# Kernel tuning notes

Hardware: AMD Instinct MI355X
Metric: run time of the kernel (lower is better)

Reference implementation:

```python
import jax, jax.numpy as jnp
import numpy as np

N = 50000      # nodes
E = 800000     # edges
IN = 128       # in_dim
EMB = 32       # emb_dim
ED = 8         # edge_dim
L = 4          # num_layers
B = 64         # num graphs in batch
OUT = 10       # out_dim
EPS = 1e-5


def setup_inputs() -> dict:
    key = jax.random.key(0)
    ks = jax.random.split(key, 16)
    f32 = jnp.float32
    def nrm(k, shape, scale):
        return jax.random.normal(k, shape, dtype=f32) * scale
    inp = {}
    inp['x'] = nrm(ks[0], (N, IN), 1.0)
    inp['edge_index'] = jax.random.randint(ks[1], (2, E), 0, N)
    inp['edge_attr'] = nrm(ks[2], (E, ED), 1.0)
    inp['batch'] = jnp.sort(jax.random.randint(ks[3], (N,), 0, B))
    # lin_in
    inp['lin_in_w'] = nrm(ks[4], (IN, EMB), 0.05)
    inp['lin_in_b'] = jnp.zeros((EMB,), f32)
    # per-layer message MLP: Linear(2e+ed->e), BN, ReLU, Linear(e->e), BN, ReLU
    inp['msg_w1'] = nrm(ks[5], (L, 2 * EMB + ED, EMB), 0.1)
    inp['msg_b1'] = jnp.zeros((L, EMB), f32)
    inp['msg_g1'] = jnp.ones((L, EMB), f32)
    inp['msg_be1'] = jnp.zeros((L, EMB), f32)
    inp['msg_w2'] = nrm(ks[6], (L, EMB, EMB), 0.1)
    inp['msg_b2'] = jnp.zeros((L, EMB), f32)
    inp['msg_g2'] = jnp.ones((L, EMB), f32)
    inp['msg_be2'] = jnp.zeros((L, EMB), f32)
    # per-layer update MLP: Linear(2e->e), BN, ReLU, Linear(e->e), BN, ReLU
    inp['upd_w1'] = nrm(ks[7], (L, 2 * EMB, EMB), 0.1)
    inp['upd_b1'] = jnp.zeros((L, EMB), f32)
    inp['upd_g1'] = jnp.ones((L, EMB), f32)
    inp['upd_be1'] = jnp.zeros((L, EMB), f32)
    inp['upd_w2'] = nrm(ks[8], (L, EMB, EMB), 0.1)
    inp['upd_b2'] = jnp.zeros((L, EMB), f32)
    inp['upd_g2'] = jnp.ones((L, EMB), f32)
    inp['upd_be2'] = jnp.zeros((L, EMB), f32)
    # lin_pred
    inp['pred_w'] = nrm(ks[9], (EMB, OUT), 0.1)
    inp['pred_b'] = jnp.zeros((OUT,), f32)
    return inp


def _bn(x, g, b):
    # BatchNorm1d in training mode: batch stats over dim 0 (biased variance)
    mu = jnp.mean(x, axis=0)
    var = jnp.mean(jnp.square(x - mu), axis=0)
    return (x - mu) * jax.lax.rsqrt(var + EPS) * g + b


def reference(x, edge_attr, lin_in_w, lin_in_b,
              msg_w1, msg_b1, msg_g1, msg_be1, msg_w2, msg_b2, msg_g2, msg_be2,
              upd_w1, upd_b1, upd_g1, upd_be1, upd_w2, upd_b2, upd_g2, upd_be2,
              pred_w, pred_b, edge_index, batch):
    src = edge_index[0]  # h_j source nodes
    dst = edge_index[1]  # h_i target nodes (aggregation index)
    h = x @ lin_in_w + lin_in_b  # [N, EMB]
    for i in range(L):
        # message: gather + concat + MLP(BN,ReLU)x2 over edges
        msg_in = jnp.concatenate([h[dst], h[src], edge_attr], axis=-1)  # [E, 2e+ed]
        m = jax.nn.relu(_bn(msg_in @ msg_w1[i] + msg_b1[i], msg_g1[i], msg_be1[i]))
        m = jax.nn.relu(_bn(m @ msg_w2[i] + msg_b2[i], msg_g2[i], msg_be2[i]))
        # aggregate: scatter-add by destination
        aggr = jax.ops.segment_sum(m, dst, num_segments=N)  # [N, EMB]
        # update: concat + MLP(BN,ReLU)x2
        u = jnp.concatenate([h, aggr], axis=-1)  # [N, 2e]
        u = jax.nn.relu(_bn(u @ upd_w1[i] + upd_b1[i], upd_g1[i], upd_be1[i]))
        u = jax.nn.relu(_bn(u @ upd_w2[i] + upd_b2[i], upd_g2[i], upd_be2[i]))
        h = u + h  # residual in MPNNModel.get_embeddings
    # global mean pool
    sums = jax.ops.segment_sum(h, batch, num_segments=B)
    counts = jax.ops.segment_sum(jnp.ones((N,), h.dtype), batch, num_segments=B)
    h_graph = sums / jnp.maximum(counts, 1.0)[:, None]
    return h_graph @ pred_w + pred_b  # [B, OUT]
```

## Files before the change

kernel.cpp:

```cpp
#include <hip/hip_runtime.h>
#include <cstddef>

#define N_NODES 50000
#define N_EDGES 800000
#define IN_DIM  128
#define EMB     32
#define ED      8
#define NLAYERS 4
#define NB      64
#define OUTD    10
#define EPS_BN  1e-5f

#define EDGE_GRID 3125
#define NODE_GRID 196
#define NODE4_GRID 782
#define AGGR_GRID 6250
#define MSG1_EPT  2
#define MSG1_GRID 1563
#define NT16      50000
#define MSG2_TPW  16
#define MSG2_GRID 782

#define SREP 4

typedef short bf16x8 __attribute__((ext_vector_type(8)));
typedef float f32x4  __attribute__((ext_vector_type(4)));


__device__ __forceinline__ unsigned short f2bf(float x) {
  union { float f; unsigned u; } v; v.f = x;
  unsigned b = v.u + 0x7FFFu + ((v.u >> 16) & 1u);
  return (unsigned short)(b >> 16);
}
__device__ __forceinline__ float bf2f(unsigned short s) {
  union { unsigned u; float f; } v; v.u = ((unsigned)s) << 16;
  return v.f;
}

__device__ __forceinline__ uint4 pack8_bf16(const float v[8]) {
  uint4 o;
  o.x = (unsigned)f2bf(v[0]) | ((unsigned)f2bf(v[1]) << 16);
  o.y = (unsigned)f2bf(v[2]) | ((unsigned)f2bf(v[3]) << 16);
  o.z = (unsigned)f2bf(v[4]) | ((unsigned)f2bf(v[5]) << 16);
  o.w = (unsigned)f2bf(v[6]) | ((unsigned)f2bf(v[7]) << 16);
  return o;
}

__device__ __forceinline__ void mac8_f4(float acc[8], const float4 v, const float* __restrict__ wk) {
#pragma unroll
  for (int j = 0; j < 8; ++j) acc[j] = fmaf(v.x, wk[j], acc[j]);
#pragma unroll
  for (int j = 0; j < 8; ++j) acc[j] = fmaf(v.y, wk[EMB + j], acc[j]);
#pragma unroll
  for (int j = 0; j < 8; ++j) acc[j] = fmaf(v.z, wk[2*EMB + j], acc[j]);
#pragma unroll
  for (int j = 0; j < 8; ++j) acc[j] = fmaf(v.w, wk[3*EMB + j], acc[j]);
}

__device__ __forceinline__ void coef_from_stats(const float* __restrict__ stats_stage,
                                                const float* __restrict__ g,
                                                const float* __restrict__ be,
                                                float inv_count, float* __restrict__ cf) {
  if (threadIdx.x < EMB) {
    const int c = threadIdx.x;
    float s = 0.f, ss = 0.f;
#pragma unroll
    for (int r = 0; r < SREP; ++r) {
      s  += stats_stage[r*64 + c];
      ss += stats_stage[r*64 + EMB + c];
    }
    const float mu  = s * inv_count;
    const float var = ss * inv_count - mu*mu;
    const float a = g[c] * rsqrtf(var + EPS_BN);
    cf[c] = a;
    cf[EMB + c] = fmaf(-mu, a, be[c]);
  }
  __syncthreads();
}

__device__ __forceinline__ void wave_stats_atomic(float ts[8], float tss[8],
                                                  float* __restrict__ lds_s,
                                                  float* __restrict__ lds_q,
                                                  float* __restrict__ stats_stage) {
  const int lane = threadIdx.x & 63;
  const int wv   = threadIdx.x >> 6;
#pragma unroll
  for (int j = 0; j < 8; ++j) {
    float a = ts[j], b = tss[j];
#pragma unroll
    for (int o = 32; o > 0; o >>= 1) {
      a += __shfl_down(a, o, 64);
      b += __shfl_down(b, o, 64);
    }
    ts[j] = a; tss[j] = b;
  }
  if (lane == 0) {
#pragma unroll
    for (int j = 0; j < 8; ++j) {
      lds_s[wv*8 + j] = ts[j];
      lds_q[wv*8 + j] = tss[j];
    }
  }
  __syncthreads();
  if (threadIdx.x < 64) {
    const float v = (threadIdx.x < 32) ? lds_s[threadIdx.x] : lds_q[threadIdx.x - 32];
    atomicAdd(stats_stage + ((blockIdx.x & (SREP-1)) << 6) + threadIdx.x, v);
  }
}

__device__ __forceinline__ void block_stats_atomic(const float ts[EMB], const float tss[EMB],
                                                   float* __restrict__ stats_stage) {
  __shared__ float sred[256];
  const int lane = threadIdx.x & 63;
  const int wid  = threadIdx.x >> 6;
#pragma unroll
  for (int c = 0; c < EMB; ++c) {
    float a = ts[c];
    float q = tss[c];
#pragma unroll
    for (int o = 32; o > 0; o >>= 1) {
      a += __shfl_down(a, o, 64);
      q += __shfl_down(q, o, 64);
    }
    if (lane == 0) { sred[wid*64 + c] = a; sred[wid*64 + EMB + c] = q; }
  }
  __syncthreads();
  if (threadIdx.x < 64) {
    const float v = sred[threadIdx.x] + sred[64 + threadIdx.x] +
                    sred[128 + threadIdx.x] + sred[192 + threadIdx.x];
    atomicAdd(stats_stage + ((blockIdx.x & (SREP-1)) << 6) + threadIdx.x, v);
  }
}


__global__ __launch_bounds__(256) void k_lin_in_pq(
    const float* __restrict__ x, const float* __restrict__ w, const float* __restrict__ b,
    const float* __restrict__ w1, const float* __restrict__ b1,
    float* __restrict__ h, unsigned short* __restrict__ p, unsigned short* __restrict__ q)
{
  __shared__ float lds_h[64][33];
  const int lane = threadIdx.x & 63;
  const int wv   = threadIdx.x >> 6;
  const int n  = blockIdx.x*64 + lane;
  const int c0 = wv*8;
  if (n < N_NODES) {
    float acc[8];
#pragma unroll
    for (int j = 0; j < 8; ++j) acc[j] = b[c0 + j];
    const float4* xp = (const float4*)(x + (size_t)n*IN_DIM);
#pragma unroll 8
    for (int k4 = 0; k4 < IN_DIM/4; ++k4)
      mac8_f4(acc, xp[k4], w + (k4*4)*EMB + c0);
    float4 o0, o1;
    o0.x = acc[0]; o0.y = acc[1]; o0.z = acc[2]; o0.w = acc[3];
    o1.x = acc[4]; o1.y = acc[5]; o1.z = acc[6]; o1.w = acc[7];
    *(float4*)(h + (size_t)n*EMB + c0)     = o0;
    *(float4*)(h + (size_t)n*EMB + c0 + 4) = o1;
#pragma unroll
    for (int j = 0; j < 8; ++j) lds_h[lane][c0 + j] = acc[j];
  }
  __syncthreads();
  if (n < N_NODES) {
    float ap[8], aq[8];
#pragma unroll
    for (int j = 0; j < 8; ++j) { ap[j] = b1[c0 + j]; aq[j] = 0.f; }
#pragma unroll
    for (int k = 0; k < EMB; ++k) {
      const float hv = lds_h[lane][k];
      const float* wp = w1 + k*EMB + c0;
      const float* wq = w1 + (EMB + k)*EMB + c0;
#pragma unroll
      for (int j = 0; j < 8; ++j) ap[j] = fmaf(hv, wp[j], ap[j]);
#pragma unroll
      for (int j = 0; j < 8; ++j) aq[j] = fmaf(hv, wq[j], aq[j]);
    }
    *(uint4*)(p + (size_t)n*EMB + c0) = pack8_bf16(ap);
    *(uint4*)(q + (size_t)n*EMB + c0) = pack8_bf16(aq);
  }
}

__global__ __launch_bounds__(256) void k_upd1(
    const float* __restrict__ h, float* __restrict__ aggr,
    const float* __restrict__ w, const float* __restrict__ b,
    float* __restrict__ stats)
{
  __shared__ float lds_s[32], lds_q[32];
  const int lane = threadIdx.x & 63;
  const int wv   = threadIdx.x >> 6;
  const int n  = blockIdx.x*64 + lane;
  const int c0 = wv*8;
  float acc[8];
#pragma unroll
  for (int j = 0; j < 8; ++j) acc[j] = 0.f;
  if (n < N_NODES) {
#pragma unroll
    for (int j = 0; j < 8; ++j) acc[j] = b[c0 + j];
    const float4* hp = (const float4*)(h + (size_t)n*EMB);
    const float4* ap = (const float4*)(aggr + (size_t)n*EMB);
#pragma unroll
    for (int k4 = 0; k4 < 8; ++k4) mac8_f4(acc, hp[k4], w + (k4*4)*EMB + c0);
#pragma unroll
    for (int k4 = 0; k4 < 8; ++k4) mac8_f4(acc, ap[k4], w + (EMB + k4*4)*EMB + c0);
  }
  float ts[8], tss[8];
#pragma unroll
  for (int j = 0; j < 8; ++j) { ts[j] = acc[j]; tss[j] = acc[j]*acc[j]; }
  wave_stats_atomic(ts, tss, lds_s, lds_q, stats);
  if (n < N_NODES) {
    float4 o0, o1;
    o0.x = acc[0]; o0.y = acc[1]; o0.z = acc[2]; o0.w = acc[3];
    o1.x = acc[4]; o1.y = acc[5]; o1.z = acc[6]; o1.w = acc[7];
    *(float4*)(aggr + (size_t)n*EMB + c0)     = o0;
    *(float4*)(aggr + (size_t)n*EMB + c0 + 4) = o1;
  }
}

__global__ __launch_bounds__(256) void k_upd2(
    float* __restrict__ z,
    const float* __restrict__ stats1, const float* __restrict__ g1, const float* __restrict__ be1,
    const float* __restrict__ w, const float* __restrict__ b,
    float* __restrict__ stats2)
{
  __shared__ float cf[64];
  __shared__ float lds_s[32], lds_q[32];
  coef_from_stats(stats1, g1, be1, 1.0f/(float)N_NODES, cf);

  const int lane = threadIdx.x & 63;
  const int wv   = threadIdx.x >> 6;
  const int n  = blockIdx.x*64 + lane;
  const int c0 = wv*8;
  float acc[8];
#pragma unroll
  for (int j = 0; j < 8; ++j) acc[j] = 0.f;
  if (n < N_NODES) {
#pragma unroll
    for (int j = 0; j < 8; ++j) acc[j] = b[c0 + j];
    const float4* zp = (const float4*)(z + (size_t)n*EMB);
#pragma unroll
    for (int k4 = 0; k4 < 8; ++k4) {
      const float4 v = zp[k4];
      const float mv[4] = {v.x, v.y, v.z, v.w};
#pragma unroll
      for (int t = 0; t < 4; ++t) {
        const int k = 4*k4 + t;
        const float m = fmaxf(fmaf(cf[k], mv[t], cf[EMB + k]), 0.f);
        const float* wk = w + k*EMB + c0;
#pragma unroll
        for (int j = 0; j < 8; ++j) acc[j] = fmaf(m, wk[j], acc[j]);
      }
    }
  }
  float ts[8], tss[8];
#pragma unroll
  for (int j = 0; j < 8; ++j) { ts[j] = acc[j]; tss[j] = acc[j]*acc[j]; }
  wave_stats_atomic(ts, tss, lds_s, lds_q, stats2);
  if (n < N_NODES) {
    float4 o0, o1;
    o0.x = acc[0]; o0.y = acc[1]; o0.z = acc[2]; o0.w = acc[3];
    o1.x = acc[4]; o1.y = acc[5]; o1.z = acc[6]; o1.w = acc[7];
    *(float4*)(z + (size_t)n*EMB + c0)     = o0;
    *(float4*)(z + (size_t)n*EMB + c0 + 4) = o1;
  }
}

__global__ __launch_bounds__(256) void k_resid_pq(
    float* __restrict__ h, const float* __restrict__ z,
    const float* __restrict__ stats, const float* __restrict__ g, const float* __restrict__ be,
    const float* __restrict__ w1_next, const float* __restrict__ b1_next,
    unsigned short* __restrict__ p, unsigned short* __restrict__ q)
{
  __shared__ float cf[64];
  __shared__ float lds_h[64][33];
  coef_from_stats(stats, g, be, 1.0f/(float)N_NODES, cf);

  const int lane = threadIdx.x & 63;
  const int wv   = threadIdx.x >> 6;
  const int n  = blockIdx.x*64 + lane;
  const int c0 = wv*8;
  if (n < N_NODES) {
    const float4* zp = (const float4*)(z + (size_t)n*EMB + c0);
    float4* hp = (float4*)(h + (size_t)n*EMB + c0);
    float hn[8];
    const float4 z0 = zp[0], z1 = zp[1];
    const float4 h0 = hp[0], h1 = hp[1];
    const float zv[8] = {z0.x, z0.y, z0.z, z0.w, z1.x, z1.y, z1.z, z1.w};
    const float hv[8] = {h0.x, h0.y, h0.z, h0.w, h1.x, h1.y, h1.z, h1.w};
#pragma unroll
    for (int j = 0; j < 8; ++j) {
      const int k = c0 + j;
      hn[j] = hv[j] + fmaxf(fmaf(cf[k], zv[j], cf[EMB + k]), 0.f);
      lds_h[lane][k] = hn[j];
    }
    float4 o0, o1;
    o0.x = hn[0]; o0.y = hn[1]; o0.z = hn[2]; o0.w = hn[3];
    o1.x = hn[4]; o1.y = hn[5]; o1.z = hn[6]; o1.w = hn[7];
    hp[0] = o0; hp[1] = o1;
  }
  __syncthreads();
  if (n < N_NODES && w1_next) {
    float ap[8], aq[8];
#pragma unroll
    for (int j = 0; j < 8; ++j) { ap[j] = b1_next[c0 + j]; aq[j] = 0.f; }
#pragma unroll
    for (int k = 0; k < EMB; ++k) {
      const float hvv = lds_h[lane][k];
      const float* wp = w1_next + k*EMB + c0;
      const float* wq = w1_next + (EMB + k)*EMB + c0;
#pragma unroll
      for (int j = 0; j < 8; ++j) ap[j] = fmaf(hvv, wp[j], ap[j]);
#pragma unroll
      for (int j = 0; j < 8; ++j) aq[j] = fmaf(hvv, wq[j], aq[j]);
    }
    *(uint4*)(p + (size_t)n*EMB + c0) = pack8_bf16(ap);
    *(uint4*)(q + (size_t)n*EMB + c0) = pack8_bf16(aq);
  }
}

__global__ __launch_bounds__(256) void k_hist(const int* __restrict__ ei, int* __restrict__ cnt) {
  const int e = blockIdx.x*256 + threadIdx.x;
  if (e < N_EDGES) atomicAdd(&cnt[ei[N_EDGES + e]], 1);
}

__global__ __launch_bounds__(256) void k_scan_a(const int* __restrict__ cnt,
                                                int* __restrict__ row_ptr, int* __restrict__ bsum) {
  __shared__ int s[256];
  const int gid = blockIdx.x*256 + threadIdx.x;
  const int v = (gid < N_NODES) ? cnt[gid] : 0;
  s[threadIdx.x] = v;
  __syncthreads();
  for (int o = 1; o < 256; o <<= 1) {
    const int t = (threadIdx.x >= o) ? s[threadIdx.x - o] : 0;
    __syncthreads();
    s[threadIdx.x] += t;
    __syncthreads();
  }
  if (gid < N_NODES) row_ptr[gid] = s[threadIdx.x] - v;
  if (threadIdx.x == 255) bsum[blockIdx.x] = s[255];
}

__global__ __launch_bounds__(256) void k_scan_b(int* __restrict__ bsum, int* __restrict__ row_ptr) {
  __shared__ int s[256];
  const int v = (threadIdx.x < NODE_GRID) ? bsum[threadIdx.x] : 0;
  s[threadIdx.x] = v;
  __syncthreads();
  for (int o = 1; o < 256; o <<= 1) {
    const int t = (threadIdx.x >= o) ? s[threadIdx.x - o] : 0;
    __syncthreads();
    s[threadIdx.x] += t;
    __syncthreads();
  }
  if (threadIdx.x < NODE_GRID) bsum[threadIdx.x] = s[threadIdx.x] - v;
  if (threadIdx.x == 0) row_ptr[N_NODES] = N_EDGES;
}

__global__ __launch_bounds__(256) void k_scan_c(int* __restrict__ row_ptr, const int* __restrict__ bsum) {
  const int gid = blockIdx.x*256 + threadIdx.x;
  if (gid < N_NODES) row_ptr[gid] += bsum[blockIdx.x];
}

__global__ __launch_bounds__(256) void k_place(const int* __restrict__ ei,
                                               const int* __restrict__ row_ptr,
                                               int* __restrict__ cnt2, int* __restrict__ perm) {
  const int e = blockIdx.x*256 + threadIdx.x;
  if (e >= N_EDGES) return;
  const int d = ei[N_EDGES + e];
  const int pos = row_ptr[d] + atomicAdd(&cnt2[d], 1);
  perm[pos] = e;
}

__global__ __launch_bounds__(256) void k_permute(
    const int* __restrict__ perm, const int* __restrict__ ei, const float* __restrict__ ea,
    int* __restrict__ src_perm, int* __restrict__ dst_perm, unsigned short* __restrict__ ea_perm)
{
  const int i = blockIdx.x*256 + threadIdx.x;
  const int e = perm[i];
  src_perm[i] = ei[e];
  dst_perm[i] = ei[N_EDGES + e];
  const float4* src4 = (const float4*)(ea + (size_t)e*ED);
  const float4 v0 = src4[0], v1 = src4[1];
  const float ev[8] = {v0.x, v0.y, v0.z, v0.w, v1.x, v1.y, v1.z, v1.w};
  unsigned u[4];
#pragma unroll
  for (int j = 0; j < 4; ++j)
    u[j] = (unsigned)f2bf(ev[2*j]) | ((unsigned)f2bf(ev[2*j+1]) << 16);
  uint4 o; o.x = u[0]; o.y = u[1]; o.z = u[2]; o.w = u[3];
  *(uint4*)(ea_perm + (size_t)i*ED) = o;
}


__global__ __launch_bounds__(256) void k_msg1(
    const unsigned short* __restrict__ pb, const unsigned short* __restrict__ qb,
    const int* __restrict__ src_perm, const int* __restrict__ dst_perm,
    const unsigned short* __restrict__ ea_perm,
    const float* __restrict__ w1b,
    unsigned short* __restrict__ y, float* __restrict__ stats)
{
  float ts[EMB], tss[EMB];
#pragma unroll
  for (int c = 0; c < EMB; ++c) { ts[c] = 0.f; tss[c] = 0.f; }
  const int base = blockIdx.x*(256*MSG1_EPT) + threadIdx.x;
  for (int it = 0; it < MSG1_EPT; ++it) {
    const int i = base + it*256;
    if (i >= N_EDGES) break;
    const int dst = dst_perm[i];
    const int src = src_perm[i];
    float acc[EMB];
    const uint4* pd = (const uint4*)(pb + (size_t)dst*EMB);
    const uint4* qs = (const uint4*)(qb + (size_t)src*EMB);
#pragma unroll
    for (int j4 = 0; j4 < 4; ++j4) {
      const uint4 a = pd[j4];
      const uint4 b = qs[j4];
      const unsigned ua[4] = {a.x, a.y, a.z, a.w};
      const unsigned ub[4] = {b.x, b.y, b.z, b.w};
#pragma unroll
      for (int t = 0; t < 4; ++t) {
        acc[j4*8 + 2*t]   = bf2f((unsigned short)(ua[t] & 0xFFFFu)) +
                            bf2f((unsigned short)(ub[t] & 0xFFFFu));
        acc[j4*8 + 2*t+1] = bf2f((unsigned short)(ua[t] >> 16)) +
                            bf2f((unsigned short)(ub[t] >> 16));
      }
    }
    const uint4 eraw = *(const uint4*)(ea_perm + (size_t)i*ED);
    const unsigned ue[4] = {eraw.x, eraw.y, eraw.z, eraw.w};
    float ev[8];
#pragma unroll
    for (int t = 0; t < 4; ++t) {
      ev[2*t]   = bf2f((unsigned short)(ue[t] & 0xFFFFu));
      ev[2*t+1] = bf2f((unsigned short)(ue[t] >> 16));
    }
#pragma unroll
    for (int k = 0; k < 8; ++k) {
      const float* wk = w1b + k*EMB;
#pragma unroll
      for (int c = 0; c < EMB; ++c) acc[c] = fmaf(ev[k], wk[c], acc[c]);
    }

    unsigned short us[EMB];
#pragma unroll
    for (int c = 0; c < EMB; ++c) us[c] = f2bf(acc[c]);
    unsigned u[16];
#pragma unroll
    for (int j = 0; j < 16; ++j)
      u[j] = (unsigned)us[2*j] | ((unsigned)us[2*j+1] << 16);
    uint4* dp = (uint4*)(y + (size_t)i*EMB);
#pragma unroll
    for (int j = 0; j < 4; ++j) {
      uint4 o; o.x = u[4*j]; o.y = u[4*j+1]; o.z = u[4*j+2]; o.w = u[4*j+3];
      dp[j] = o;
    }
#pragma unroll
    for (int c = 0; c < EMB; ++c) {
      const float v = bf2f(us[c]);
      ts[c] += v;
      tss[c] = fmaf(v, v, tss[c]);
    }
  }
  block_stats_atomic(ts, tss, stats);
}

__global__ __launch_bounds__(256) void k_msg2(
    unsigned short* __restrict__ y,
    const float* __restrict__ stats1, const float* __restrict__ g1, const float* __restrict__ be1,
    const float* __restrict__ w2, const float* __restrict__ b2,
    float* __restrict__ stats2)
{
  __shared__ __align__(16) unsigned short lds_t[4][16*32];
  __shared__ float lds_s[4][32], lds_q[4][32];
  __shared__ float cf[64];

  coef_from_stats(stats1, g1, be1, 1.0f/(float)N_EDGES, cf);

  const int lane = threadIdx.x & 63;
  const int wid  = threadIdx.x >> 6;
  const int n0 = lane & 15;
  const int kb = lane >> 4;

  bf16x8 Blo, Bhi;
#pragma unroll
  for (int j = 0; j < 8; ++j) {
    Blo[j] = (short)f2bf(w2[(kb*8 + j)*EMB + n0]);
    Bhi[j] = (short)f2bf(w2[(kb*8 + j)*EMB + 16 + n0]);
  }
  float a1[8], c1[8];
#pragma unroll
  for (int j = 0; j < 8; ++j) {
    a1[j] = cf[kb*8 + j];
    c1[j] = cf[EMB + kb*8 + j];
  }
  const float b2c0 = b2[n0], b2c1 = b2[16 + n0];

  float ts[8], tss[8];
#pragma unroll
  for (int j = 0; j < 8; ++j) { ts[j] = 0.f; tss[j] = 0.f; }

  const int tile0 = blockIdx.x * (MSG2_TPW*4);
  for (int t = 0; t < MSG2_TPW; ++t) {
    const int tile = tile0 + t*4 + wid;
    if (tile >= NT16) break;
    const size_t e0 = (size_t)tile * 16;

    const uint4 araw = *(const uint4*)(y + (e0 + n0)*EMB + kb*8);
    unsigned int ua[4] = {araw.x, araw.y, araw.z, araw.w};
    bf16x8 A;
#pragma unroll
    for (int j = 0; j < 4; ++j) {
      float v0 = bf2f((unsigned short)(ua[j] & 0xFFFFu));
      float v1 = bf2f((unsigned short)(ua[j] >> 16));
      v0 = fmaxf(fmaf(a1[2*j],   v0, c1[2*j]),   0.f);
      v1 = fmaxf(fmaf(a1[2*j+1], v1, c1[2*j+1]), 0.f);
      A[2*j]   = (short)f2bf(v0);
      A[2*j+1] = (short)f2bf(v1);
    }

    f32x4 acc0 = {0.f, 0.f, 0.f, 0.f};
    f32x4 acc1 = {0.f, 0.f, 0.f, 0.f};
    acc0 = __builtin_amdgcn_mfma_f32_16x16x32_bf16(A, Blo, acc0, 0, 0, 0);
    acc1 = __builtin_amdgcn_mfma_f32_16x16x32_bf16(A, Bhi, acc1, 0, 0, 0);

#pragma unroll
    for (int r = 0; r < 4; ++r) {
      const int row = kb*4 + r;
      lds_t[wid][row*32 + n0]      = f2bf(acc0[r] + b2c0);
      lds_t[wid][row*32 + 16 + n0] = f2bf(acc1[r] + b2c1);
    }
    const uint4 orow = *(const uint4*)&lds_t[wid][(lane>>2)*32 + (lane&3)*8];
    *(uint4*)(y + (e0 + (lane>>2))*EMB + (lane&3)*8) = orow;

    unsigned int uo[4] = {orow.x, orow.y, orow.z, orow.w};
#pragma unroll
    for (int j = 0; j < 4; ++j) {
      const float v0 = bf2f((unsigned short)(uo[j] & 0xFFFFu));
      const float v1 = bf2f((unsigned short)(uo[j] >> 16));
      ts[2*j]   += v0;  tss[2*j]   = fmaf(v0, v0, tss[2*j]);
      ts[2*j+1] += v1;  tss[2*j+1] = fmaf(v1, v1, tss[2*j+1]);
    }
  }

#pragma unroll
  for (int j = 0; j < 8; ++j) {
    float s = ts[j], qq = tss[j];
#pragma unroll
    for (int o = 4; o < 64; o <<= 1) {
      s  += __shfl_xor(s, o, 64);
      qq += __shfl_xor(qq, o, 64);
    }
    ts[j] = s; tss[j] = qq;
  }
  if (lane < 4) {
#pragma unroll
    for (int j = 0; j < 8; ++j) {
      lds_s[wid][lane*8 + j] = ts[j];
      lds_q[wid][lane*8 + j] = tss[j];
    }
  }
  __syncthreads();
  if (threadIdx.x < 64) {
    const int c = threadIdx.x & 31;
    const int kind = threadIdx.x >> 5;
    float v = 0.f;
#pragma unroll
    for (int wq = 0; wq < 4; ++wq)
      v += kind ? lds_q[wq][c] : lds_s[wq][c];
    atomicAdd(stats2 + ((blockIdx.x & (SREP-1)) << 6) + kind*32 + c, v);
  }
}

__global__ __launch_bounds__(256) void k_aggr(
    const unsigned short* __restrict__ y, const int* __restrict__ row_ptr,
    const float* __restrict__ stats2, const float* __restrict__ g2, const float* __restrict__ be2,
    float* __restrict__ aggr)
{
  __shared__ float cf[64];
  coef_from_stats(stats2, g2, be2, 1.0f/(float)N_EDGES, cf);

  const int grp = threadIdx.x >> 5;
  const int l   = threadIdx.x & 31;
  const int rof = l >> 4;
  const int cp  = l & 15;
  const int n = blockIdx.x*8 + grp;
  if (n >= N_NODES) return;
  const float a0 = cf[2*cp],     b0 = cf[EMB + 2*cp];
  const float a1 = cf[2*cp + 1], b1 = cf[EMB + 2*cp + 1];
  const int lo = row_ptr[n], hi = row_ptr[n+1];
  float s0 = 0.f, s1 = 0.f;
  for (int i = lo + rof; i < hi; i += 2) {
    const unsigned u = *(const unsigned*)(y + (size_t)i*EMB + 2*cp);
    const float v0 = bf2f((unsigned short)(u & 0xFFFFu));
    const float v1 = bf2f((unsigned short)(u >> 16));
    s0 += fmaxf(fmaf(a0, v0, b0), 0.f);
    s1 += fmaxf(fmaf(a1, v1, b1), 0.f);
  }
  s0 += __shfl_xor(s0, 16, 64);
  s1 += __shfl_xor(s1, 16, 64);
  if (rof == 0) {
    float2 o; o.x = s0; o.y = s1;
    *(float2*)(aggr + (size_t)n*EMB + 2*cp) = o;
  }
}

__global__ void k_pool(const float* __restrict__ h, const int* __restrict__ batch,
                       const float* __restrict__ pw, const float* __restrict__ pb,
                       float* __restrict__ out)
{
  __shared__ float sred[256];
  __shared__ float hg[EMB];
  const int b = blockIdx.x;
  int lo = 0, hi = N_NODES;
  while (lo < hi) { int m = (lo + hi) >> 1; if (batch[m] < b) lo = m + 1; else hi = m; }
  const int start = lo;
  hi = N_NODES;
  while (lo < hi) { int m = (lo + hi) >> 1; if (batch[m] < b + 1) lo = m + 1; else hi = m; }
  const int end = lo;

  const int c = threadIdx.x & (EMB-1);
  const int r = threadIdx.x >> 5;
  float s = 0.f;
  for (int n = start + r; n < end; n += 8) s += h[(size_t)n*EMB + c];
  sred[threadIdx.x] = s;
  __syncthreads();
  if (threadIdx.x < EMB) {
    float tot = 0.f;
#pragma unroll
    for (int r2 = 0; r2 < 8; ++r2) tot += sred[r2*EMB + threadIdx.x];
    const float cnt = (float)(end - start);
    hg[threadIdx.x] = tot / fmaxf(cnt, 1.f);
  }
  __syncthreads();
  if (threadIdx.x < OUTD) {
    float acc = pb[threadIdx.x];
#pragma unroll
    for (int cc = 0; cc < EMB; ++cc) acc = fmaf(hg[cc], pw[cc*OUTD + threadIdx.x], acc);
    out[b*OUTD + threadIdx.x] = acc;
  }
}


extern "C" void kernel_launch(void* const* d_in, const int* in_sizes, int n_in,
                              void* d_out, int out_size, void* d_ws, size_t ws_size,
                              hipStream_t stream) {
  const float* x        = (const float*)d_in[0];
  const int*   ei       = (const int*)  d_in[1];
  const float* ea       = (const float*)d_in[2];
  const int*   batch    = (const int*)  d_in[3];
  const float* lin_in_w = (const float*)d_in[4];
  const float* lin_in_b = (const float*)d_in[5];
  const float* msg_w1   = (const float*)d_in[6];
  const float* msg_b1   = (const float*)d_in[7];
  const float* msg_g1   = (const float*)d_in[8];
  const float* msg_be1  = (const float*)d_in[9];
  const float* msg_w2   = (const float*)d_in[10];
  const float* msg_b2   = (const float*)d_in[11];
  const float* msg_g2   = (const float*)d_in[12];
  const float* msg_be2  = (const float*)d_in[13];
  const float* upd_w1   = (const float*)d_in[14];
  const float* upd_b1   = (const float*)d_in[15];
  const float* upd_g1   = (const float*)d_in[16];
  const float* upd_be1  = (const float*)d_in[17];
  const float* upd_w2   = (const float*)d_in[18];
  const float* upd_b2   = (const float*)d_in[19];
  const float* upd_g2   = (const float*)d_in[20];
  const float* upd_be2  = (const float*)d_in[21];
  const float* pred_w   = (const float*)d_in[22];
  const float* pred_b   = (const float*)d_in[23];
  float* out = (float*)d_out;

  char* wsb = (char*)d_ws;
  unsigned short* y  = (unsigned short*)wsb;
  unsigned short* eap= (unsigned short*)(wsb + (size_t)N_EDGES*EMB*2);
  unsigned short* p  = eap + (size_t)N_EDGES*ED;
  unsigned short* q  = p + (size_t)N_NODES*EMB;
  float* h       = (float*)(q + (size_t)N_NODES*EMB);
  float* aggr    = h + (size_t)N_NODES*EMB;
  float* stats   = aggr + (size_t)N_NODES*EMB;
  int*   cnt     = (int*)(stats + 16*SREP*64);
  int*   cnt2    = cnt + N_NODES;
  int*   row_ptr = cnt2 + N_NODES;
  int*   bsum    = row_ptr + N_NODES + 1;
  int*   perm    = bsum + 256;
  int*   src_perm= perm + N_EDGES;
  int*   dst_perm= src_perm + N_EDGES;
  const size_t need = ((size_t)((char*)(dst_perm + N_EDGES) - wsb));
  if (ws_size < need) return;

  hipMemsetAsync(stats, 0, (16*SREP*64 + 2*N_NODES)*sizeof(float), stream);

  k_lin_in_pq<<<NODE4_GRID, 256, 0, stream>>>(x, lin_in_w, lin_in_b, msg_w1, msg_b1, h, p, q);
  k_hist<<<EDGE_GRID, 256, 0, stream>>>(ei, cnt);
  k_scan_a<<<NODE_GRID, 256, 0, stream>>>(cnt, row_ptr, bsum);
  k_scan_b<<<1, 256, 0, stream>>>(bsum, row_ptr);
  k_scan_c<<<NODE_GRID, 256, 0, stream>>>(row_ptr, bsum);
  k_place<<<EDGE_GRID, 256, 0, stream>>>(ei, row_ptr, cnt2, perm);
  k_permute<<<EDGE_GRID, 256, 0, stream>>>(perm, ei, ea, src_perm, dst_perm, eap);

  for (int l = 0; l < NLAYERS; ++l) {
    const int st = l*4;
    const float* w1  = msg_w1 + (size_t)l*(2*EMB+ED)*EMB;
    const float* w1b = w1 + (size_t)2*EMB*EMB;
    const float* w2  = msg_w2 + (size_t)l*EMB*EMB;
    const float* uw1 = upd_w1 + (size_t)l*(2*EMB)*EMB;
    const float* uw2 = upd_w2 + (size_t)l*EMB*EMB;
    const float* w1_next = (l+1 < NLAYERS) ? msg_w1 + (size_t)(l+1)*(2*EMB+ED)*EMB : nullptr;
    const float* b1_next = (l+1 < NLAYERS) ? msg_b1 + (size_t)(l+1)*EMB : nullptr;

    k_msg1<<<MSG1_GRID, 256, 0, stream>>>(p, q, src_perm, dst_perm, eap,
                                          w1b, y, stats + (size_t)st*SREP*64);
    k_msg2<<<MSG2_GRID, 256, 0, stream>>>(y, stats + (size_t)st*SREP*64,
                                          msg_g1 + l*EMB, msg_be1 + l*EMB,
                                          w2, msg_b2 + l*EMB, stats + (size_t)(st+1)*SREP*64);
    k_aggr<<<AGGR_GRID, 256, 0, stream>>>(y, row_ptr, stats + (size_t)(st+1)*SREP*64,
                                          msg_g2 + l*EMB, msg_be2 + l*EMB, aggr);
    k_upd1<<<NODE4_GRID, 256, 0, stream>>>(h, aggr, uw1, upd_b1 + l*EMB,
                                           stats + (size_t)(st+2)*SREP*64);
    k_upd2<<<NODE4_GRID, 256, 0, stream>>>(aggr, stats + (size_t)(st+2)*SREP*64,
                                           upd_g1 + l*EMB, upd_be1 + l*EMB,
                                           uw2, upd_b2 + l*EMB, stats + (size_t)(st+3)*SREP*64);
    k_resid_pq<<<NODE4_GRID, 256, 0, stream>>>(h, aggr, stats + (size_t)(st+3)*SREP*64,
                                               upd_g2 + l*EMB, upd_be2 + l*EMB,
                                               w1_next, b1_next, p, q);
  }

  k_pool<<<NB, 256, 0, stream>>>(h, batch, pred_w, pred_b, out);
}
```

Measured before the change: 951.7 us.

## Fuse aggregation with update linear, merge preprocessing kernels, use MFMA for lin_in

Measured after the change: 883.9 us. 7.1% less time.

```diff
diff --git a/kernel.cpp b/kernel.cpp
--- a/kernel.cpp
+++ b/kernel.cpp
@@ -14,10 +14,12 @@
 #define EDGE_GRID 3125
 #define NODE_GRID 196
 #define NODE4_GRID 782
-#define AGGR_GRID 6250
+#define AU_GRID   6250
 #define MSG1_EPT  2
 #define MSG1_GRID 1563
 #define NT16      50000
+#define NTILE_N   3125
+#define LIN_GRID  782
 #define MSG2_TPW  16
 #define MSG2_GRID 782
 
@@ -35,26 +37,6 @@
 __device__ __forceinline__ float bf2f(unsigned short s) {
   union { unsigned u; float f; } v; v.u = ((unsigned)s) << 16;
   return v.f;
-}
-
-__device__ __forceinline__ uint4 pack8_bf16(const float v[8]) {
-  uint4 o;
-  o.x = (unsigned)f2bf(v[0]) | ((unsigned)f2bf(v[1]) << 16);
-  o.y = (unsigned)f2bf(v[2]) | ((unsigned)f2bf(v[3]) << 16);
-  o.z = (unsigned)f2bf(v[4]) | ((unsigned)f2bf(v[5]) << 16);
-  o.w = (unsigned)f2bf(v[6]) | ((unsigned)f2bf(v[7]) << 16);
-  return o;
-}
-
-__device__ __forceinline__ void mac8_f4(float acc[8], const float4 v, const float* __restrict__ wk) {
-#pragma unroll
-  for (int j = 0; j < 8; ++j) acc[j] = fmaf(v.x, wk[j], acc[j]);
-#pragma unroll
-  for (int j = 0; j < 8; ++j) acc[j] = fmaf(v.y, wk[EMB + j], acc[j]);
-#pragma unroll
-  for (int j = 0; j < 8; ++j) acc[j] = fmaf(v.z, wk[2*EMB + j], acc[j]);
-#pragma unroll
-  for (int j = 0; j < 8; ++j) acc[j] = fmaf(v.w, wk[3*EMB + j], acc[j]);
 }
 
 __device__ __forceinline__ void coef_from_stats(const float* __restrict__ stats_stage,
@@ -78,6 +60,30 @@
   __syncthreads();
 }
 
+__device__ __forceinline__ void block_stats_atomic(const float ts[EMB], const float tss[EMB],
+                                                   float* __restrict__ stats_stage) {
+  __shared__ float sred[256];
+  const int lane = threadIdx.x & 63;
+  const int wid  = threadIdx.x >> 6;
+#pragma unroll
+  for (int c = 0; c < EMB; ++c) {
+    float a = ts[c];
+    float q = tss[c];
+#pragma unroll
+    for (int o = 32; o > 0; o >>= 1) {
+      a += __shfl_down(a, o, 64);
+      q += __shfl_down(q, o, 64);
+    }
+    if (lane == 0) { sred[wid*64 + c] = a; sred[wid*64 + EMB + c] = q; }
+  }
+  __syncthreads();
+  if (threadIdx.x < 64) {
+    const float v = sred[threadIdx.x] + sred[64 + threadIdx.x] +
+                    sred[128 + threadIdx.x] + sred[192 + threadIdx.x];
+    atomicAdd(stats_stage + ((blockIdx.x & (SREP-1)) << 6) + threadIdx.x, v);
+  }
+}
+
 __device__ __forceinline__ void wave_stats_atomic(float ts[8], float tss[8],
                                                   float* __restrict__ lds_s,
                                                   float* __restrict__ lds_q,
@@ -108,110 +114,412 @@
   }
 }
 
-__device__ __forceinline__ void block_stats_atomic(const float ts[EMB], const float tss[EMB],
-                                                   float* __restrict__ stats_stage) {
-  __shared__ float sred[256];
+__device__ __forceinline__ void mac8_f4(float acc[8], const float4 v, const float* wk) {
+#pragma unroll
+  for (int j = 0; j < 8; ++j) acc[j] = fmaf(v.x, wk[j], acc[j]);
+#pragma unroll
+  for (int j = 0; j < 8; ++j) acc[j] = fmaf(v.y, wk[EMB + j], acc[j]);
+#pragma unroll
+  for (int j = 0; j < 8; ++j) acc[j] = fmaf(v.z, wk[2*EMB + j], acc[j]);
+#pragma unroll
+  for (int j = 0; j < 8; ++j) acc[j] = fmaf(v.w, wk[3*EMB + j], acc[j]);
+}
+
+#define HSTRIDE 40
+
+__global__ __launch_bounds__(256) void k_lin_in_pq(
+    const float* __restrict__ x, const float* __restrict__ w, const float* __restrict__ b,
+    const float* __restrict__ w1, const float* __restrict__ b1, const int* __restrict__ ei,
+    float* __restrict__ h, unsigned short* __restrict__ p, unsigned short* __restrict__ q,
+    int* __restrict__ cnt)
+{
+  __shared__ __align__(16) unsigned short lds_hb[4][16*HSTRIDE];
+  __shared__ __align__(16) unsigned short lds_pq[4][16*HSTRIDE];
+  const int lane = threadIdx.x & 63;
+  const int wv   = threadIdx.x >> 6;
+  const int n0i  = lane & 15;
+  const int quad = lane >> 4;
+
+  const int tile = blockIdx.x*4 + wv;
+  if (tile < NTILE_N) {
+    const int r0 = tile*16;
+    bf16x8 BwL[4], BwH[4];
+#pragma unroll
+    for (int kb = 0; kb < 4; ++kb) {
+#pragma unroll
+      for (int j = 0; j < 8; ++j) {
+        const int k = kb*32 + quad*8 + j;
+        BwL[kb][j] = (short)f2bf(w[k*EMB + n0i]);
+        BwH[kb][j] = (short)f2bf(w[k*EMB + 16 + n0i]);
+      }
+    }
+    f32x4 accL = {0.f,0.f,0.f,0.f};
+    f32x4 accH = {0.f,0.f,0.f,0.f};
+#pragma unroll
+    for (int kb = 0; kb < 4; ++kb) {
+      const float4 xa = *(const float4*)(x + (size_t)(r0 + n0i)*IN_DIM + kb*32 + quad*8);
+      const float4 xb = *(const float4*)(x + (size_t)(r0 + n0i)*IN_DIM + kb*32 + quad*8 + 4);
+      bf16x8 A;
+      A[0] = (short)f2bf(xa.x); A[1] = (short)f2bf(xa.y);
+      A[2] = (short)f2bf(xa.z); A[3] = (short)f2bf(xa.w);
+      A[4] = (short)f2bf(xb.x); A[5] = (short)f2bf(xb.y);
+      A[6] = (short)f2bf(xb.z); A[7] = (short)f2bf(xb.w);
+      accL = __builtin_amdgcn_mfma_f32_16x16x32_bf16(A, BwL[kb], accL, 0, 0, 0);
+      accH = __builtin_amdgcn_mfma_f32_16x16x32_bf16(A, BwH[kb], accH, 0, 0, 0);
+    }
+    const float bL = b[n0i], bH = b[16 + n0i];
+#pragma unroll
+    for (int r = 0; r < 4; ++r) {
+      const int row = quad*4 + r;
+      const float vL = accL[r] + bL;
+      const float vH = accH[r] + bH;
+      h[(size_t)(r0 + row)*EMB + n0i]      = vL;
+      h[(size_t)(r0 + row)*EMB + 16 + n0i] = vH;
+      lds_hb[wv][row*HSTRIDE + n0i]      = f2bf(vL);
+      lds_hb[wv][row*HSTRIDE + 16 + n0i] = f2bf(vH);
+    }
+    bf16x8 A2;
+#pragma unroll
+    for (int j = 0; j < 8; ++j)
+      A2[j] = (short)lds_hb[wv][n0i*HSTRIDE + quad*8 + j];
+    bf16x8 BpL, BpH, BqL, BqH;
+#pragma unroll
+    for (int j = 0; j < 8; ++j) {
+      const int k = quad*8 + j;
+      BpL[j] = (short)f2bf(w1[k*EMB + n0i]);
+      BpH[j] = (short)f2bf(w1[k*EMB + 16 + n0i]);
+      BqL[j] = (short)f2bf(w1[(EMB + k)*EMB + n0i]);
+      BqH[j] = (short)f2bf(w1[(EMB + k)*EMB + 16 + n0i]);
+    }
+    const f32x4 z4 = {0.f,0.f,0.f,0.f};
+    f32x4 pL = __builtin_amdgcn_mfma_f32_16x16x32_bf16(A2, BpL, z4, 0, 0, 0);
+    f32x4 pH = __builtin_amdgcn_mfma_f32_16x16x32_bf16(A2, BpH, z4, 0, 0, 0);
+    f32x4 qL = __builtin_amdgcn_mfma_f32_16x16x32_bf16(A2, BqL, z4, 0, 0, 0);
+    f32x4 qH = __builtin_amdgcn_mfma_f32_16x16x32_bf16(A2, BqH, z4, 0, 0, 0);
+    const float b1L = b1[n0i], b1H = b1[16 + n0i];
+#pragma unroll
+    for (int r = 0; r < 4; ++r) {
+      const int row = quad*4 + r;
+      lds_pq[wv][row*HSTRIDE + n0i]      = f2bf(pL[r] + b1L);
+      lds_pq[wv][row*HSTRIDE + 16 + n0i] = f2bf(pH[r] + b1H);
+    }
+    {
+      const int row2 = lane >> 2;
+      const int c8   = (lane & 3)*8;
+      const uint4 ov = *(const uint4*)&lds_pq[wv][row2*HSTRIDE + c8];
+      *(uint4*)(p + (size_t)(r0 + row2)*EMB + c8) = ov;
+    }
+#pragma unroll
+    for (int r = 0; r < 4; ++r) {
+      const int row = quad*4 + r;
+      lds_pq[wv][row*HSTRIDE + n0i]      = f2bf(qL[r]);
+      lds_pq[wv][row*HSTRIDE + 16 + n0i] = f2bf(qH[r]);
+    }
+    {
+      const int row2 = lane >> 2;
+      const int c8   = (lane & 3)*8;
+      const uint4 ov = *(const uint4*)&lds_pq[wv][row2*HSTRIDE + c8];
+      *(uint4*)(q + (size_t)(r0 + row2)*EMB + c8) = ov;
+    }
+  }
+  for (int e = blockIdx.x*256 + threadIdx.x; e < N_EDGES; e += gridDim.x*256)
+    atomicAdd(&cnt[ei[N_EDGES + e]], 1);
+}
+
+__global__ __launch_bounds__(256) void k_scan_a(const int* __restrict__ cnt,
+                                                int* __restrict__ row_ptr, int* __restrict__ bsum) {
+  __shared__ int s[256];
+  const int gid = blockIdx.x*256 + threadIdx.x;
+  const int v = (gid < N_NODES) ? cnt[gid] : 0;
+  s[threadIdx.x] = v;
+  __syncthreads();
+  for (int o = 1; o < 256; o <<= 1) {
+    const int t = (threadIdx.x >= o) ? s[threadIdx.x - o] : 0;
+    __syncthreads();
+    s[threadIdx.x] += t;
+    __syncthreads();
+  }
+  if (gid < N_NODES) row_ptr[gid] = s[threadIdx.x] - v;
+  if (threadIdx.x == 255) bsum[blockIdx.x] = s[255];
+}
+
+__global__ __launch_bounds__(256) void k_scan_bc(int* __restrict__ row_ptr,
+                                                 const int* __restrict__ bsum) {
+  __shared__ int s[256];
+  const int t = threadIdx.x;
+  const int v = (t < NODE_GRID) ? bsum[t] : 0;
+  s[t] = v;
+  __syncthreads();
+  for (int o = 1; o < 256; o <<= 1) {
+    const int tt = (t >= o) ? s[t - o] : 0;
+    __syncthreads();
+    s[t] += tt;
+    __syncthreads();
+  }
+  const int off = (blockIdx.x == 0) ? 0 : s[blockIdx.x - 1];
+  const int gid = blockIdx.x*256 + t;
+  if (gid < N_NODES) row_ptr[gid] += off;
+  if (blockIdx.x == 0 && t == 0) row_ptr[N_NODES] = N_EDGES;
+}
+
+__global__ __launch_bounds__(256) void k_place_scatter(
+    const int* __restrict__ ei, const float* __restrict__ ea,
+    const int* __restrict__ row_ptr, int* __restrict__ cnt2,
+    int* __restrict__ src_perm, int* __restrict__ dst_perm,
+    unsigned short* __restrict__ ea_perm)
+{
+  const int e = blockIdx.x*256 + threadIdx.x;
+  const int d = ei[N_EDGES + e];
+  const int pos = row_ptr[d] + atomicAdd(&cnt2[d], 1);
+  src_perm[pos] = ei[e];
+  dst_perm[pos] = d;
+  const float4 v0 = ((const float4*)(ea + (size_t)e*ED))[0];
+  const float4 v1 = ((const float4*)(ea + (size_t)e*ED))[1];
+  const float ev[8] = {v0.x, v0.y, v0.z, v0.w, v1.x, v1.y, v1.z, v1.w};
+  unsigned u[4];
+#pragma unroll
+  for (int j = 0; j < 4; ++j)
+    u[j] = (unsigned)f2bf(ev[2*j]) | ((unsigned)f2bf(ev[2*j+1]) << 16);
+  uint4 o; o.x = u[0]; o.y = u[1]; o.z = u[2]; o.w = u[3];
+  *(uint4*)(ea_perm + (size_t)pos*ED) = o;
+}
+
+
+__global__ __launch_bounds__(256) void k_msg1(
+    const unsigned short* __restrict__ pb, const unsigned short* __restrict__ qb,
+    const int* __restrict__ src_perm, const int* __restrict__ dst_perm,
+    const unsigned short* __restrict__ ea_perm,
+    const float* __restrict__ w1b,
+    unsigned short* __restrict__ y, float* __restrict__ stats)
+{
+  float ts[EMB], tss[EMB];
+#pragma unroll
+  for (int c = 0; c < EMB; ++c) { ts[c] = 0.f; tss[c] = 0.f; }
+  const int base = blockIdx.x*(256*MSG1_EPT) + threadIdx.x;
+  for (int it = 0; it < MSG1_EPT; ++it) {
+    const int i = base + it*256;
+    if (i >= N_EDGES) break;
+    const int dst = dst_perm[i];
+    const int src = src_perm[i];
+    float acc[EMB];
+    const uint4* pd = (const uint4*)(pb + (size_t)dst*EMB);
+    const uint4* qs = (const uint4*)(qb + (size_t)src*EMB);
+#pragma unroll
+    for (int j4 = 0; j4 < 4; ++j4) {
+      const uint4 a = pd[j4];
+      const uint4 b = qs[j4];
+      const unsigned ua[4] = {a.x, a.y, a.z, a.w};
+      const unsigned ub[4] = {b.x, b.y, b.z, b.w};
+#pragma unroll
+      for (int t = 0; t < 4; ++t) {
+        acc[j4*8 + 2*t]   = bf2f((unsigned short)(ua[t] & 0xFFFFu)) +
+                            bf2f((unsigned short)(ub[t] & 0xFFFFu));
+        acc[j4*8 + 2*t+1] = bf2f((unsigned short)(ua[t] >> 16)) +
+                            bf2f((unsigned short)(ub[t] >> 16));
+      }
+    }
+    const uint4 eraw = *(const uint4*)(ea_perm + (size_t)i*ED);
+    const unsigned ue[4] = {eraw.x, eraw.y, eraw.z, eraw.w};
+    float ev[8];
+#pragma unroll
+    for (int t = 0; t < 4; ++t) {
+      ev[2*t]   = bf2f((unsigned short)(ue[t] & 0xFFFFu));
+      ev[2*t+1] = bf2f((unsigned short)(ue[t] >> 16));
+    }
+#pragma unroll
+    for (int k = 0; k < 8; ++k) {
+      const float* wk = w1b + k*EMB;
+#pragma unroll
+      for (int c = 0; c < EMB; ++c) acc[c] = fmaf(ev[k], wk[c], acc[c]);
+    }
+    unsigned short us[EMB];
+#pragma unroll
+    for (int c = 0; c < EMB; ++c) us[c] = f2bf(acc[c]);
+    unsigned u[16];
+#pragma unroll
+    for (int j = 0; j < 16; ++j)
+      u[j] = (unsigned)us[2*j] | ((unsigned)us[2*j+1] << 16);
+    uint4* dp = (uint4*)(y + (size_t)i*EMB);
+#pragma unroll
+    for (int j = 0; j < 4; ++j) {
+      uint4 o; o.x = u[4*j]; o.y = u[4*j+1]; o.z = u[4*j+2]; o.w = u[4*j+3];
+      dp[j] = o;
+    }
+#pragma unroll
+    for (int c = 0; c < EMB; ++c) {
+      const float v = bf2f(us[c]);
+      ts[c] += v;
+      tss[c] = fmaf(v, v, tss[c]);
+    }
+  }
+  block_stats_atomic(ts, tss, stats);
+}
+
+__global__ __launch_bounds__(256) void k_msg2(
+    unsigned short* __restrict__ y,
+    const float* __restrict__ stats1, const float* __restrict__ g1, const float* __restrict__ be1,
+    const float* __restrict__ w2, const float* __restrict__ b2,
+    float* __restrict__ stats2)
+{
+  __shared__ __align__(16) unsigned short lds_t[4][16*32];
+  __shared__ float lds_s[4][32], lds_q[4][32];
+  __shared__ float cf[64];
+
+  coef_from_stats(stats1, g1, be1, 1.0f/(float)N_EDGES, cf);
+
   const int lane = threadIdx.x & 63;
   const int wid  = threadIdx.x >> 6;
-#pragma unroll
-  for (int c = 0; c < EMB; ++c) {
-    float a = ts[c];
-    float q = tss[c];
-#pragma unroll
-    for (int o = 32; o > 0; o >>= 1) {
-      a += __shfl_down(a, o, 64);
-      q += __shfl_down(q, o, 64);
-    }
-    if (lane == 0) { sred[wid*64 + c] = a; sred[wid*64 + EMB + c] = q; }
+  const int n0 = lane & 15;
+  const int kb = lane >> 4;
+
+  bf16x8 Blo, Bhi;
+#pragma unroll
+  for (int j = 0; j < 8; ++j) {
+    Blo[j] = (short)f2bf(w2[(kb*8 + j)*EMB + n0]);
+    Bhi[j] = (short)f2bf(w2[(kb*8 + j)*EMB + 16 + n0]);
+  }
+  float a1[8], c1[8];
+#pragma unroll
+  for (int j = 0; j < 8; ++j) {
+    a1[j] = cf[kb*8 + j];
+    c1[j] = cf[EMB + kb*8 + j];
+  }
+  const float b2c0 = b2[n0], b2c1 = b2[16 + n0];
+
+  float ts[8], tss[8];
+#pragma unroll
+  for (int j = 0; j < 8; ++j) { ts[j] = 0.f; tss[j] = 0.f; }
+
+  const int tile0 = blockIdx.x * (MSG2_TPW*4);
+  for (int t = 0; t < MSG2_TPW; ++t) {
+    const int tile = tile0 + t*4 + wid;
+    if (tile >= NT16) break;
+    const size_t e0 = (size_t)tile * 16;
+
+    const uint4 araw = *(const uint4*)(y + (e0 + n0)*EMB + kb*8);
+    unsigned int ua[4] = {araw.x, araw.y, araw.z, araw.w};
+    bf16x8 A;
+#pragma unroll
+    for (int j = 0; j < 4; ++j) {
+      float v0 = bf2f((unsigned short)(ua[j] & 0xFFFFu));
+      float v1 = bf2f((unsigned short)(ua[j] >> 16));
+      v0 = fmaxf(fmaf(a1[2*j],   v0, c1[2*j]),   0.f);
+      v1 = fmaxf(fmaf(a1[2*j+1], v1, c1[2*j+1]), 0.f);
+      A[2*j]   = (short)f2bf(v0);
+      A[2*j+1] = (short)f2bf(v1);
+    }
+
+    f32x4 acc0 = {0.f, 0.f, 0.f, 0.f};
+    f32x4 acc1 = {0.f, 0.f, 0.f, 0.f};
+    acc0 = __builtin_amdgcn_mfma_f32_16x16x32_bf16(A, Blo, acc0, 0, 0, 0);
+    acc1 = __builtin_amdgcn_mfma_f32_16x16x32_bf16(A, Bhi, acc1, 0, 0, 0);
+
+#pragma unroll
+    for (int r = 0; r < 4; ++r) {
+      const int row = kb*4 + r;
+      lds_t[wid][row*32 + n0]      = f2bf(acc0[r] + b2c0);
+      lds_t[wid][row*32 + 16 + n0] = f2bf(acc1[r] + b2c1);
+    }
+    const uint4 orow = *(const uint4*)&lds_t[wid][(lane>>2)*32 + (lane&3)*8];
+    *(uint4*)(y + (e0 + (lane>>2))*EMB + (lane&3)*8) = orow;
+
+    unsigned int uo[4] = {orow.x, orow.y, orow.z, orow.w};
+#pragma unroll
+    for (int j = 0; j < 4; ++j) {
+      const float v0 = bf2f((unsigned short)(uo[j] & 0xFFFFu));
+      const float v1 = bf2f((unsigned short)(uo[j] >> 16));
+      ts[2*j]   += v0;  tss[2*j]   = fmaf(v0, v0, tss[2*j]);
+      ts[2*j+1] += v1;  tss[2*j+1] = fmaf(v1, v1, tss[2*j+1]);
+    }
+  }
+
+#pragma unroll
+  for (int j = 0; j < 8; ++j) {
+    float s = ts[j], qq = tss[j];
+#pragma unroll
+    for (int o = 4; o < 64; o <<= 1) {
+      s  += __shfl_xor(s, o, 64);
+      qq += __shfl_xor(qq, o, 64);
+    }
+    ts[j] = s; tss[j] = qq;
+  }
+  if (lane < 4) {
+#pragma unroll
+    for (int j = 0; j < 8; ++j) {
+      lds_s[wid][lane*8 + j] = ts[j];
+      lds_q[wid][lane*8 + j] = tss[j];
+    }
   }
   __syncthreads();
   if (threadIdx.x < 64) {
-    const float v = sred[threadIdx.x] + sred[64 + threadIdx.x] +
-                    sred[128 + threadIdx.x] + sred[192 + threadIdx.x];
-    atomicAdd(stats_stage + ((blockIdx.x & (SREP-1)) << 6) + threadIdx.x, v);
-  }
-}
-
-
-__global__ __launch_bounds__(256) void k_lin_in_pq(
-    const float* __restrict__ x, const float* __restrict__ w, const float* __restrict__ b,
-    const float* __restrict__ w1, const float* __restrict__ b1,
-    float* __restrict__ h, unsigned short* __restrict__ p, unsigned short* __restrict__ q)
+    const int c = threadIdx.x & 31;
+    const int kind = threadIdx.x >> 5;
+    float v = 0.f;
+#pragma unroll
+    for (int wq = 0; wq < 4; ++wq)
+      v += kind ? lds_q[wq][c] : lds_s[wq][c];
+    atomicAdd(stats2 + ((blockIdx.x & (SREP-1)) << 6) + kind*32 + c, v);
+  }
+}
+
+__global__ __launch_bounds__(256) void k_aggr_upd1(
+    const unsigned short* __restrict__ y, const int* __restrict__ row_ptr,
+    const float* __restrict__ h,
+    const float* __restrict__ stats1, const float* __restrict__ g2, const float* __restrict__ be2,
+    const float* __restrict__ uw1, const float* __restrict__ ub1,
+    float* __restrict__ z, float* __restrict__ stats2)
 {
-  __shared__ float lds_h[64][33];
-  const int lane = threadIdx.x & 63;
-  const int wv   = threadIdx.x >> 6;
-  const int n  = blockIdx.x*64 + lane;
-  const int c0 = wv*8;
-  if (n < N_NODES) {
-    float acc[8];
-#pragma unroll
-    for (int j = 0; j < 8; ++j) acc[j] = b[c0 + j];
-    const float4* xp = (const float4*)(x + (size_t)n*IN_DIM);
-#pragma unroll 8
-    for (int k4 = 0; k4 < IN_DIM/4; ++k4)
-      mac8_f4(acc, xp[k4], w + (k4*4)*EMB + c0);
-    float4 o0, o1;
-    o0.x = acc[0]; o0.y = acc[1]; o0.z = acc[2]; o0.w = acc[3];
-    o1.x = acc[4]; o1.y = acc[5]; o1.z = acc[6]; o1.w = acc[7];
-    *(float4*)(h + (size_t)n*EMB + c0)     = o0;
-    *(float4*)(h + (size_t)n*EMB + c0 + 4) = o1;
-#pragma unroll
-    for (int j = 0; j < 8; ++j) lds_h[lane][c0 + j] = acc[j];
-  }
-  __syncthreads();
-  if (n < N_NODES) {
-    float ap[8], aq[8];
-#pragma unroll
-    for (int j = 0; j < 8; ++j) { ap[j] = b1[c0 + j]; aq[j] = 0.f; }
-#pragma unroll
-    for (int k = 0; k < EMB; ++k) {
-      const float hv = lds_h[lane][k];
-      const float* wp = w1 + k*EMB + c0;
-      const float* wq = w1 + (EMB + k)*EMB + c0;
-#pragma unroll
-      for (int j = 0; j < 8; ++j) ap[j] = fmaf(hv, wp[j], ap[j]);
-#pragma unroll
-      for (int j = 0; j < 8; ++j) aq[j] = fmaf(hv, wq[j], aq[j]);
-    }
-    *(uint4*)(p + (size_t)n*EMB + c0) = pack8_bf16(ap);
-    *(uint4*)(q + (size_t)n*EMB + c0) = pack8_bf16(aq);
-  }
-}
-
-__global__ __launch_bounds__(256) void k_upd1(
-    const float* __restrict__ h, float* __restrict__ aggr,
-    const float* __restrict__ w, const float* __restrict__ b,
-    float* __restrict__ stats)
-{
-  __shared__ float lds_s[32], lds_q[32];
-  const int lane = threadIdx.x & 63;
-  const int wv   = threadIdx.x >> 6;
-  const int n  = blockIdx.x*64 + lane;
-  const int c0 = wv*8;
-  float acc[8];
-#pragma unroll
-  for (int j = 0; j < 8; ++j) acc[j] = 0.f;
-  if (n < N_NODES) {
-#pragma unroll
-    for (int j = 0; j < 8; ++j) acc[j] = b[c0 + j];
-    const float4* hp = (const float4*)(h + (size_t)n*EMB);
-    const float4* ap = (const float4*)(aggr + (size_t)n*EMB);
-#pragma unroll
-    for (int k4 = 0; k4 < 8; ++k4) mac8_f4(acc, hp[k4], w + (k4*4)*EMB + c0);
-#pragma unroll
-    for (int k4 = 0; k4 < 8; ++k4) mac8_f4(acc, ap[k4], w + (EMB + k4*4)*EMB + c0);
-  }
-  float ts[8], tss[8];
-#pragma unroll
-  for (int j = 0; j < 8; ++j) { ts[j] = acc[j]; tss[j] = acc[j]*acc[j]; }
-  wave_stats_atomic(ts, tss, lds_s, lds_q, stats);
-  if (n < N_NODES) {
-    float4 o0, o1;
-    o0.x = acc[0]; o0.y = acc[1]; o0.z = acc[2]; o0.w = acc[3];
-    o1.x = acc[4]; o1.y = acc[5]; o1.z = acc[6]; o1.w = acc[7];
-    *(float4*)(aggr + (size_t)n*EMB + c0)     = o0;
-    *(float4*)(aggr + (size_t)n*EMB + c0 + 4) = o1;
+  __shared__ float cf[64];
+  __shared__ float lh[8][32];
+  __shared__ float la[8][32];
+  __shared__ float rs[4][32], rq[4][32];
+  coef_from_stats(stats1, g2, be2, 1.0f/(float)N_EDGES, cf);
+
+  const int g = threadIdx.x >> 5;
+  const int l = threadIdx.x & 31;
+  const int n = blockIdx.x*8 + g;
+
+  lh[g][l] = h[(size_t)n*EMB + l];
+
+  const int rof = l >> 4;
+  const int cp  = l & 15;
+  const float a0 = cf[2*cp],     b0 = cf[EMB + 2*cp];
+  const float a1 = cf[2*cp + 1], b1 = cf[EMB + 2*cp + 1];
+  const int lo = row_ptr[n], hi = row_ptr[n+1];
+  float s0 = 0.f, s1 = 0.f;
+  for (int i = lo + rof; i < hi; i += 2) {
+    const unsigned u = *(const unsigned*)(y + (size_t)i*EMB + 2*cp);
+    const float v0 = bf2f((unsigned short)(u & 0xFFFFu));
+    const float v1 = bf2f((unsigned short)(u >> 16));
+    s0 += fmaxf(fmaf(a0, v0, b0), 0.f);
+    s1 += fmaxf(fmaf(a1, v1, b1), 0.f);
+  }
+  s0 += __shfl_xor(s0, 16, 64);
+  s1 += __shfl_xor(s1, 16, 64);
+  if (rof == 0) { la[g][2*cp] = s0; la[g][2*cp + 1] = s1; }
+  __syncthreads();
+
+  float acc = ub1[l];
+#pragma unroll
+  for (int k = 0; k < EMB; ++k) acc = fmaf(lh[g][k], uw1[k*EMB + l], acc);
+#pragma unroll
+  for (int k = 0; k < EMB; ++k) acc = fmaf(la[g][k], uw1[(EMB + k)*EMB + l], acc);
+  z[(size_t)n*EMB + l] = acc;
+
+  const float sq = acc*acc;
+  const float a2 = acc + __shfl_down(acc, 32, 64);
+  const float q2 = sq  + __shfl_down(sq,  32, 64);
+  const int wv = threadIdx.x >> 6;
+  if ((threadIdx.x & 63) < 32) { rs[wv][l] = a2; rq[wv][l] = q2; }
+  __syncthreads();
+  if (threadIdx.x < 64) {
+    const int c = threadIdx.x & 31;
+    const int kind = threadIdx.x >> 5;
+    float v = 0.f;
+#pragma unroll
+    for (int wq = 0; wq < 4; ++wq)
+      v += kind ? rq[wq][c] : rs[wq][c];
+    atomicAdd(stats2 + ((blockIdx.x & (SREP-1)) << 6) + kind*32 + c, v);
   }
 }
 
@@ -311,291 +619,16 @@
 #pragma unroll
       for (int j = 0; j < 8; ++j) aq[j] = fmaf(hvv, wq[j], aq[j]);
     }
-    *(uint4*)(p + (size_t)n*EMB + c0) = pack8_bf16(ap);
-    *(uint4*)(q + (size_t)n*EMB + c0) = pack8_bf16(aq);
-  }
-}
-
-__global__ __launch_bounds__(256) void k_hist(const int* __restrict__ ei, int* __restrict__ cnt) {
-  const int e = blockIdx.x*256 + threadIdx.x;
-  if (e < N_EDGES) atomicAdd(&cnt[ei[N_EDGES + e]], 1);
-}
-
-__global__ __launch_bounds__(256) void k_scan_a(const int* __restrict__ cnt,
-                                                int* __restrict__ row_ptr, int* __restrict__ bsum) {
-  __shared__ int s[256];
-  const int gid = blockIdx.x*256 + threadIdx.x;
-  const int v = (gid < N_NODES) ? cnt[gid] : 0;
-  s[threadIdx.x] = v;
-  __syncthreads();
-  for (int o = 1; o < 256; o <<= 1) {
-    const int t = (threadIdx.x >= o) ? s[threadIdx.x - o] : 0;
-    __syncthreads();
-    s[threadIdx.x] += t;
-    __syncthreads();
-  }
-  if (gid < N_NODES) row_ptr[gid] = s[threadIdx.x] - v;
-  if (threadIdx.x == 255) bsum[blockIdx.x] = s[255];
-}
-
-__global__ __launch_bounds__(256) void k_scan_b(int* __restrict__ bsum, int* __restrict__ row_ptr) {
-  __shared__ int s[256];
-  const int v = (threadIdx.x < NODE_GRID) ? bsum[threadIdx.x] : 0;
-  s[threadIdx.x] = v;
-  __syncthreads();
-  for (int o = 1; o < 256; o <<= 1) {
-    const int t = (threadIdx.x >= o) ? s[threadIdx.x - o] : 0;
-    __syncthreads();
-    s[threadIdx.x] += t;
-    __syncthreads();
-  }
-  if (threadIdx.x < NODE_GRID) bsum[threadIdx.x] = s[threadIdx.x] - v;
-  if (threadIdx.x == 0) row_ptr[N_NODES] = N_EDGES;
-}
-
-__global__ __launch_bounds__(256) void k_scan_c(int* __restrict__ row_ptr, const int* __restrict__ bsum) {
-  const int gid = blockIdx.x*256 + threadIdx.x;
-  if (gid < N_NODES) row_ptr[gid] += bsum[blockIdx.x];
-}
-
-__global__ __launch_bounds__(256) void k_place(const int* __restrict__ ei,
-                                               const int* __restrict__ row_ptr,
-                                               int* __restrict__ cnt2, int* __restrict__ perm) {
-  const int e = blockIdx.x*256 + threadIdx.x;
-  if (e >= N_EDGES) return;
-  const int d = ei[N_EDGES + e];
-  const int pos = row_ptr[d] + atomicAdd(&cnt2[d], 1);
-  perm[pos] = e;
-}
-
-__global__ __launch_bounds__(256) void k_permute(
-    const int* __restrict__ perm, const int* __restrict__ ei, const float* __restrict__ ea,
-    int* __restrict__ src_perm, int* __restrict__ dst_perm, unsigned short* __restrict__ ea_perm)
-{
-  const int i = blockIdx.x*256 + threadIdx.x;
-  const int e = perm[i];
-  src_perm[i] = ei[e];
-  dst_perm[i] = ei[N_EDGES + e];
-  const float4* src4 = (const float4*)(ea + (size_t)e*ED);
-  const float4 v0 = src4[0], v1 = src4[1];
-  const float ev[8] = {v0.x, v0.y, v0.z, v0.w, v1.x, v1.y, v1.z, v1.w};
-  unsigned u[4];
-#pragma unroll
-  for (int j = 0; j < 4; ++j)
-    u[j] = (unsigned)f2bf(ev[2*j]) | ((unsigned)f2bf(ev[2*j+1]) << 16);
-  uint4 o; o.x = u[0]; o.y = u[1]; o.z = u[2]; o.w = u[3];
-  *(uint4*)(ea_perm + (size_t)i*ED) = o;
-}
-
-
-__global__ __launch_bounds__(256) void k_msg1(
-    const unsigned short* __restrict__ pb, const unsigned short* __restrict__ qb,
-    const int* __restrict__ src_perm, const int* __restrict__ dst_perm,
-    const unsigned short* __restrict__ ea_perm,
-    const float* __restrict__ w1b,
-    unsigned short* __restrict__ y, float* __restrict__ stats)
-{
-  float ts[EMB], tss[EMB];
-#pragma unroll
-  for (int c = 0; c < EMB; ++c) { ts[c] = 0.f; tss[c] = 0.f; }
-  const int base = blockIdx.x*(256*MSG1_EPT) + threadIdx.x;
-  for (int it = 0; it < MSG1_EPT; ++it) {
-    const int i = base + it*256;
-    if (i >= N_EDGES) break;
-    const int dst = dst_perm[i];
-    const int src = src_perm[i];
-    float acc[EMB];
-    const uint4* pd = (const uint4*)(pb + (size_t)dst*EMB);
-    const uint4* qs = (const uint4*)(qb + (size_t)src*EMB);
-#pragma unroll
-    for (int j4 = 0; j4 < 4; ++j4) {
-      const uint4 a = pd[j4];
-      const uint4 b = qs[j4];
-      const unsigned ua[4] = {a.x, a.y, a.z, a.w};
-      const unsigned ub[4] = {b.x, b.y, b.z, b.w};
-#pragma unroll
-      for (int t = 0; t < 4; ++t) {
-        acc[j4*8 + 2*t]   = bf2f((unsigned short)(ua[t] & 0xFFFFu)) +
-                            bf2f((unsigned short)(ub[t] & 0xFFFFu));
-        acc[j4*8 + 2*t+1] = bf2f((unsigned short)(ua[t] >> 16)) +
-                            bf2f((unsigned short)(ub[t] >> 16));
-      }
-    }
-    const uint4 eraw = *(const uint4*)(ea_perm + (size_t)i*ED);
-    const unsigned ue[4] = {eraw.x, eraw.y, eraw.z, eraw.w};
-    float ev[8];
-#pragma unroll
-    for (int t = 0; t < 4; ++t) {
-      ev[2*t]   = bf2f((unsigned short)(ue[t] & 0xFFFFu));
-      ev[2*t+1] = bf2f((unsigned short)(ue[t] >> 16));
-    }
-#pragma unroll
-    for (int k = 0; k < 8; ++k) {
-      const float* wk = w1b + k*EMB;
-#pragma unroll
-      for (int c = 0; c < EMB; ++c) acc[c] = fmaf(ev[k], wk[c], acc[c]);
-    }
-
-    unsigned short us[EMB];
-#pragma unroll
-    for (int c = 0; c < EMB; ++c) us[c] = f2bf(acc[c]);
-    unsigned u[16];
-#pragma unroll
-    for (int j = 0; j < 16; ++j)
-      u[j] = (unsigned)us[2*j] | ((unsigned)us[2*j+1] << 16);
-    uint4* dp = (uint4*)(y + (size_t)i*EMB);
+    unsigned up[4], uq[4];
 #pragma unroll
     for (int j = 0; j < 4; ++j) {
-      uint4 o; o.x = u[4*j]; o.y = u[4*j+1]; o.z = u[4*j+2]; o.w = u[4*j+3];
-      dp[j] = o;
-    }
-#pragma unroll
-    for (int c = 0; c < EMB; ++c) {
-      const float v = bf2f(us[c]);
-      ts[c] += v;
-      tss[c] = fmaf(v, v, tss[c]);
-    }
-  }
-  block_stats_atomic(ts, tss, stats);
-}
-
-__global__ __launch_bounds__(256) void k_msg2(
-    unsigned short* __restrict__ y,
-    const float* __restrict__ stats1, const float* __restrict__ g1, const float* __restrict__ be1,
-    const float* __restrict__ w2, const float* __restrict__ b2,
-    float* __restrict__ stats2)
-{
-  __shared__ __align__(16) unsigned short lds_t[4][16*32];
-  __shared__ float lds_s[4][32], lds_q[4][32];
-  __shared__ float cf[64];
-
-  coef_from_stats(stats1, g1, be1, 1.0f/(float)N_EDGES, cf);
-
-  const int lane = threadIdx.x & 63;
-  const int wid  = threadIdx.x >> 6;
-  const int n0 = lane & 15;
-  const int kb = lane >> 4;
-
-  bf16x8 Blo, Bhi;
-#pragma unroll
-  for (int j = 0; j < 8; ++j) {
-    Blo[j] = (short)f2bf(w2[(kb*8 + j)*EMB + n0]);
-    Bhi[j] = (short)f2bf(w2[(kb*8 + j)*EMB + 16 + n0]);
-  }
-  float a1[8], c1[8];
-#pragma unroll
-  for (int j = 0; j < 8; ++j) {
-    a1[j] = cf[kb*8 + j];
-    c1[j] = cf[EMB + kb*8 + j];
-  }
-  const float b2c0 = b2[n0], b2c1 = b2[16 + n0];
-
-  float ts[8], tss[8];
-#pragma unroll
-  for (int j = 0; j < 8; ++j) { ts[j] = 0.f; tss[j] = 0.f; }
-
-  const int tile0 = blockIdx.x * (MSG2_TPW*4);
-  for (int t = 0; t < MSG2_TPW; ++t) {
-    const int tile = tile0 + t*4 + wid;
-    if (tile >= NT16) break;
-    const size_t e0 = (size_t)tile * 16;
-
-    const uint4 araw = *(const uint4*)(y + (e0 + n0)*EMB + kb*8);
-    unsigned int ua[4] = {araw.x, araw.y, araw.z, araw.w};
-    bf16x8 A;
-#pragma unroll
-    for (int j = 0; j < 4; ++j) {
-      float v0 = bf2f((unsigned short)(ua[j] & 0xFFFFu));
-      float v1 = bf2f((unsigned short)(ua[j] >> 16));
-      v0 = fmaxf(fmaf(a1[2*j],   v0, c1[2*j]),   0.f);
-      v1 = fmaxf(fmaf(a1[2*j+1], v1, c1[2*j+1]), 0.f);
-      A[2*j]   = (short)f2bf(v0);
-      A[2*j+1] = (short)f2bf(v1);
-    }
-
-    f32x4 acc0 = {0.f, 0.f, 0.f, 0.f};
-    f32x4 acc1 = {0.f, 0.f, 0.f, 0.f};
-    acc0 = __builtin_amdgcn_mfma_f32_16x16x32_bf16(A, Blo, acc0, 0, 0, 0);
-    acc1 = __builtin_amdgcn_mfma_f32_16x16x32_bf16(A, Bhi, acc1, 0, 0, 0);
-
-#pragma unroll
-    for (int r = 0; r < 4; ++r) {
-      const int row = kb*4 + r;
-      lds_t[wid][row*32 + n0]      = f2bf(acc0[r] + b2c0);
-      lds_t[wid][row*32 + 16 + n0] = f2bf(acc1[r] + b2c1);
-    }
-    const uint4 orow = *(const uint4*)&lds_t[wid][(lane>>2)*32 + (lane&3)*8];
-    *(uint4*)(y + (e0 + (lane>>2))*EMB + (lane&3)*8) = orow;
-
-    unsigned int uo[4] = {orow.x, orow.y, orow.z, orow.w};
-#pragma unroll
-    for (int j = 0; j < 4; ++j) {
-      const float v0 = bf2f((unsigned short)(uo[j] & 0xFFFFu));
-      const float v1 = bf2f((unsigned short)(uo[j] >> 16));
-      ts[2*j]   += v0;  tss[2*j]   = fmaf(v0, v0, tss[2*j]);
-      ts[2*j+1] += v1;  tss[2*j+1] = fmaf(v1, v1, tss[2*j+1]);
-    }
-  }
-
-#pragma unroll
-  for (int j = 0; j < 8; ++j) {
-    float s = ts[j], qq = tss[j];
-#pragma unroll
-    for (int o = 4; o < 64; o <<= 1) {
-      s  += __shfl_xor(s, o, 64);
-      qq += __shfl_xor(qq, o, 64);
-    }
-    ts[j] = s; tss[j] = qq;
-  }
-  if (lane < 4) {
-#pragma unroll
-    for (int j = 0; j < 8; ++j) {
-      lds_s[wid][lane*8 + j] = ts[j];
-      lds_q[wid][lane*8 + j] = tss[j];
-    }
-  }
-  __syncthreads();
-  if (threadIdx.x < 64) {
-    const int c = threadIdx.x & 31;
-    const int kind = threadIdx.x >> 5;
-    float v = 0.f;
-#pragma unroll
-    for (int wq = 0; wq < 4; ++wq)
-      v += kind ? lds_q[wq][c] : lds_s[wq][c];
-    atomicAdd(stats2 + ((blockIdx.x & (SREP-1)) << 6) + kind*32 + c, v);
-  }
-}
-
-__global__ __launch_bounds__(256) void k_aggr(
-    const unsigned short* __restrict__ y, const int* __restrict__ row_ptr,
-    const float* __restrict__ stats2, const float* __restrict__ g2, const float* __restrict__ be2,
-    float* __restrict__ aggr)
-{
-  __shared__ float cf[64];
-  coef_from_stats(stats2, g2, be2, 1.0f/(float)N_EDGES, cf);
-
-  const int grp = threadIdx.x >> 5;
-  const int l   = threadIdx.x & 31;
-  const int rof = l >> 4;
-  const int cp  = l & 15;
-  const int n = blockIdx.x*8 + grp;
-  if (n >= N_NODES) return;
-  const float a0 = cf[2*cp],     b0 = cf[EMB + 2*cp];
-  const float a1 = cf[2*cp + 1], b1 = cf[EMB + 2*cp + 1];
-  const int lo = row_ptr[n], hi = row_ptr[n+1];
-  float s0 = 0.f, s1 = 0.f;
-  for (int i = lo + rof; i < hi; i += 2) {
-    const unsigned u = *(const unsigned*)(y + (size_t)i*EMB + 2*cp);
-    const float v0 = bf2f((unsigned short)(u & 0xFFFFu));
-    const float v1 = bf2f((unsigned short)(u >> 16));
-    s0 += fmaxf(fmaf(a0, v0, b0), 0.f);
-    s1 += fmaxf(fmaf(a1, v1, b1), 0.f);
-  }
-  s0 += __shfl_xor(s0, 16, 64);
-  s1 += __shfl_xor(s1, 16, 64);
-  if (rof == 0) {
-    float2 o; o.x = s0; o.y = s1;
-    *(float2*)(aggr + (size_t)n*EMB + 2*cp) = o;
+      up[j] = (unsigned)f2bf(ap[2*j]) | ((unsigned)f2bf(ap[2*j+1]) << 16);
+      uq[j] = (unsigned)f2bf(aq[2*j]) | ((unsigned)f2bf(aq[2*j+1]) << 16);
+    }
+    uint4 op; op.x = up[0]; op.y = up[1]; op.z = up[2]; op.w = up[3];
+    uint4 oq; oq.x = uq[0]; oq.y = uq[1]; oq.z = uq[2]; oq.w = uq[3];
+    *(uint4*)(p + (size_t)n*EMB + c0) = op;
+    *(uint4*)(q + (size_t)n*EMB + c0) = oq;
   }
 }
 
@@ -671,27 +704,25 @@
   unsigned short* p  = eap + (size_t)N_EDGES*ED;
   unsigned short* q  = p + (size_t)N_NODES*EMB;
   float* h       = (float*)(q + (size_t)N_NODES*EMB);
-  float* aggr    = h + (size_t)N_NODES*EMB;
-  float* stats   = aggr + (size_t)N_NODES*EMB;
+  float* z       = h + (size_t)N_NODES*EMB;
+  float* stats   = z + (size_t)N_NODES*EMB;
   int*   cnt     = (int*)(stats + 16*SREP*64);
   int*   cnt2    = cnt + N_NODES;
   int*   row_ptr = cnt2 + N_NODES;
   int*   bsum    = row_ptr + N_NODES + 1;
-  int*   perm    = bsum + 256;
-  int*   src_perm= perm + N_EDGES;
+  int*   src_perm= bsum + 256;
   int*   dst_perm= src_perm + N_EDGES;
   const size_t need = ((size_t)((char*)(dst_perm + N_EDGES) - wsb));
   if (ws_size < need) return;
 
   hipMemsetAsync(stats, 0, (16*SREP*64 + 2*N_NODES)*sizeof(float), stream);
 
-  k_lin_in_pq<<<NODE4_GRID, 256, 0, stream>>>(x, lin_in_w, lin_in_b, msg_w1, msg_b1, h, p, q);
-  k_hist<<<EDGE_GRID, 256, 0, stream>>>(ei, cnt);
+  k_lin_in_pq<<<LIN_GRID, 256, 0, stream>>>(x, lin_in_w, lin_in_b, msg_w1, msg_b1, ei,
+                                            h, p, q, cnt);
   k_scan_a<<<NODE_GRID, 256, 0, stream>>>(cnt, row_ptr, bsum);
-  k_scan_b<<<1, 256, 0, stream>>>(bsum, row_ptr);
-  k_scan_c<<<NODE_GRID, 256, 0, stream>>>(row_ptr, bsum);
-  k_place<<<EDGE_GRID, 256, 0, stream>>>(ei, row_ptr, cnt2, perm);
-  k_permute<<<EDGE_GRID, 256, 0, stream>>>(perm, ei, ea, src_perm, dst_perm, eap);
+  k_scan_bc<<<NODE_GRID, 256, 0, stream>>>(row_ptr, bsum);
+  k_place_scatter<<<EDGE_GRID, 256, 0, stream>>>(ei, ea, row_ptr, cnt2,
+                                                 src_perm, dst_perm, eap);
 
   for (int l = 0; l < NLAYERS; ++l) {
     const int st = l*4;
@@ -708,14 +739,15 @@
     k_msg2<<<MSG2_GRID, 256, 0, stream>>>(y, stats + (size_t)st*SREP*64,
                                           msg_g1 + l*EMB, msg_be1 + l*EMB,
                                           w2, msg_b2 + l*EMB, stats + (size_t)(st+1)*SREP*64);
-    k_aggr<<<AGGR_GRID, 256, 0, stream>>>(y, row_ptr, stats + (size_t)(st+1)*SREP*64,
-                                          msg_g2 + l*EMB, msg_be2 + l*EMB, aggr);
-    k_upd1<<<NODE4_GRID, 256, 0, stream>>>(h, aggr, uw1, upd_b1 + l*EMB,
-                                           stats + (size_t)(st+2)*SREP*64);
-    k_upd2<<<NODE4_GRID, 256, 0, stream>>>(aggr, stats + (size_t)(st+2)*SREP*64,
+    k_aggr_upd1<<<AU_GRID, 256, 0, stream>>>(y, row_ptr, h,
+                                             stats + (size_t)(st+1)*SREP*64,
+                                             msg_g2 + l*EMB, msg_be2 + l*EMB,
+                                             uw1, upd_b1 + l*EMB,
+                                             z, stats + (size_t)(st+2)*SREP*64);
+    k_upd2<<<NODE4_GRID, 256, 0, stream>>>(z, stats + (size_t)(st+2)*SREP*64,
                                            upd_g1 + l*EMB, upd_be1 + l*EMB,
                                            uw2, upd_b2 + l*EMB, stats + (size_t)(st+3)*SREP*64);
-    k_resid_pq<<<NODE4_GRID, 256, 0, stream>>>(h, aggr, stats + (size_t)(st+3)*SREP*64,
+    k_resid_pq<<<NODE4_GRID, 256, 0, stream>>>(h, z, stats + (size_t)(st+3)*SREP*64,
                                                upd_g2 + l*EMB, upd_be2 + l*EMB,
                                                w1_next, b1_next, p, q);
   }
```
